# Optimization experiments

Measured on AMD Instinct MI355X. Metric: run time of the kernel, lower is better.

Reference implementation:

```python
import jax, jax.numpy as jnp
import numpy as np

N_NODES = 100000
N_EDGES = 6400000

def setup_inputs() -> dict:
    key = jax.random.key(0)
    ks = jax.random.split(key, 12)
    x = jax.random.normal(ks[0], (N_NODES, 2), dtype=jnp.float32)
    edge_index = jax.random.randint(ks[1], (2, N_EDGES), 0, N_NODES, dtype=jnp.int32)
    def w(k, fi, fo):
        return jax.random.normal(k, (fi, fo), dtype=jnp.float32) * (1.0 / np.sqrt(fi))
    return {
        "x": x, "edge_index": edge_index,
        "W0": w(ks[2], 2, 8), "b0": jnp.zeros((8,), jnp.float32),
        "W1": w(ks[3], 8, 8), "b1": jnp.zeros((8,), jnp.float32),
        "W2": w(ks[4], 8, 8), "b2": jnp.zeros((8,), jnp.float32),
        "W3": w(ks[5], 8, 8), "b3": jnp.zeros((8,), jnp.float32),
        "Wv": w(ks[6], 8, 1), "bv": jnp.zeros((1,), jnp.float32),
        "Wp": w(ks[7], 8, 1), "bp": jnp.zeros((1,), jnp.float32),
    }

def _gcn_norm(edge_index, n_nodes):
    # PyG GCNConv default: add self-loops, symmetric D^{-1/2} A_hat D^{-1/2}
    loops = jnp.arange(n_nodes, dtype=edge_index.dtype)
    src = jnp.concatenate([edge_index[0], loops])
    dst = jnp.concatenate([edge_index[1], loops])
    deg = jax.ops.segment_sum(jnp.ones_like(dst, dtype=jnp.float32), dst,
                              num_segments=n_nodes)
    dis = jax.lax.rsqrt(jnp.maximum(deg, 1.0))  # deg >= 1 due to self-loops
    norm = dis[src] * dis[dst]                   # [E + N]
    return src, dst, norm

def _gcn_conv(x, W, b, src, dst, norm, n_nodes):
    h = x @ W                                     # small GEMM [N, fo]
    msg = h[src] * norm[:, None]                  # gather + normalize
    out = jax.ops.segment_sum(msg, dst, num_segments=n_nodes)  # scatter-add
    return out + b

def reference(x, edge_index, W0, b0, W1, b1, W2, b2, W3, b3, Wv, bv, Wp, bp):
    n = x.shape[0]
    src, dst, norm = _gcn_norm(edge_index, n)
    h = x
    for W, b in ((W0, b0), (W1, b1), (W2, b2), (W3, b3)):
        h = jax.nn.elu(_gcn_conv(h, W, b, src, dst, norm, n))
    mean_val = _gcn_conv(h, Wv, bv, src, dst, norm, n)   # [N, 1]
    value = jnp.mean(mean_val, axis=0, keepdims=True)    # global_mean_pool, 1 graph -> [1, 1]
    proba = _gcn_conv(h, Wp, bp, src, dst, norm, n)      # [N, 1]
    return (proba, value)
```

## Files before the change

### kernel.cpp

```cpp
#include <hip/hip_runtime.h>

#define NT 256
#define CHUNK 1024
#define PBLK2 2048
#define PTILE 4096

static inline int nbi(long long n) { return (int)((n + NT - 1) / NT); }


__global__ __launch_bounds__(256) void k_histB(const int* __restrict__ dst,
                                               int* __restrict__ histB,
                                               int E, int NB) {
    __shared__ int lh[512];
    int t = threadIdx.x;
    for (int i = t; i < 512; i += 256) lh[i] = 0;
    __syncthreads();
    int chunk = (E + gridDim.x - 1) / gridDim.x;
    int lo = blockIdx.x * chunk, hi = min(E, lo + chunk);
    for (int i = lo + t; i < hi; i += 256)
        atomicAdd(&lh[dst[i] >> 8], 1);
    __syncthreads();
    for (int b = t; b < NB; b += 256)
        histB[(size_t)blockIdx.x * NB + b] = lh[b];
}

__global__ __launch_bounds__(256) void k_scanB2(const int* __restrict__ histB,
                                                int* __restrict__ cursorT,
                                                int* __restrict__ tot,
                                                int NB, int nblk) {
    __shared__ int ch[256];
    __shared__ int carry;
    int b = blockIdx.x, t = threadIdx.x;
    if (t == 0) carry = 0;
    __syncthreads();
    for (int c = 0; c < nblk; c += 256) {
        int blk = c + t;
        int v = (blk < nblk) ? histB[(size_t)blk * NB + b] : 0;
        ch[t] = v;
        __syncthreads();
        for (int o = 1; o < 256; o <<= 1) {
            int x = (t >= o) ? ch[t - o] : 0;
            __syncthreads();
            ch[t] += x;
            __syncthreads();
        }
        int excl = ch[t] - v + carry;
        if (blk < nblk) cursorT[(size_t)b * PBLK2 + blk] = excl;
        __syncthreads();
        if (t == 0) carry += ch[255];
        __syncthreads();
    }
    if (t == 0) tot[b] = carry;
}

__global__ __launch_bounds__(512) void k_bscan(const int* __restrict__ hist_g,
                                               int* __restrict__ bbase,
                                               int* __restrict__ cursor,
                                               int* __restrict__ rowst,
                                               int NB, int N, int E) {
    __shared__ int s[512];
    int t = threadIdx.x;
    int own = (t < NB) ? hist_g[t] : 0;
    s[t] = own;
    __syncthreads();
    for (int o = 1; o < 512; o <<= 1) {
        int v = (t >= o) ? s[t - o] : 0;
        __syncthreads();
        s[t] += v;
        __syncthreads();
    }
    if (t < NB) { int ex = s[t] - own; bbase[t] = ex; cursor[t] = ex; }
    if (t == 0) { bbase[NB] = E; rowst[N] = E; }
}

__global__ __launch_bounds__(256) void k_partF(const int* __restrict__ src,
                                               const int* __restrict__ dst,
                                               const int* __restrict__ bbase,
                                               const int* __restrict__ cursorT,
                                               int* __restrict__ part,
                                               int E, int NB) {
    __shared__ int wcur[512];
    __shared__ int th[512], tloff[512], tcnt[512];
    __shared__ int ps[256];
    __shared__ int stage[PTILE];
    __shared__ unsigned short sbkt[PTILE];
    int t = threadIdx.x;
    int chunk = (E + gridDim.x - 1) / gridDim.x;
    int lo = blockIdx.x * chunk, hi = min(E, lo + chunk);
    if (lo >= hi) return;

    for (int b = t; b < NB; b += 256)
        wcur[b] = bbase[b] + cursorT[(size_t)b * PBLK2 + blockIdx.x];
    __syncthreads();

    for (int tlo = lo; tlo < hi; tlo += PTILE) {
        int thi = min(hi, tlo + PTILE);
        int cnt = thi - tlo;
        for (int i = t; i < 512; i += 256) { th[i] = 0; tcnt[i] = 0; }
        __syncthreads();
        for (int i = tlo + t; i < thi; i += 256) atomicAdd(&th[dst[i] >> 8], 1);
        __syncthreads();
        int a0 = th[2 * t], a1 = th[2 * t + 1];
        int psum = a0 + a1;
        ps[t] = psum;
        __syncthreads();
        for (int o = 1; o < 256; o <<= 1) {
            int v = (t >= o) ? ps[t - o] : 0;
            __syncthreads();
            ps[t] += v;
            __syncthreads();
        }
        int excl = ps[t] - psum;
        tloff[2 * t] = excl;
        tloff[2 * t + 1] = excl + a0;
        __syncthreads();
        for (int i = tlo + t; i < thi; i += 256) {
            int d = dst[i], s = src[i];
            int b = d >> 8;
            int pos = tloff[b] + atomicAdd(&tcnt[b], 1);
            stage[pos] = ((d & 255) << 17) | s;
            sbkt[pos] = (unsigned short)b;
        }
        __syncthreads();
        for (int i = t; i < cnt; i += 256) {
            int b = sbkt[i];
            part[wcur[b] + (i - tloff[b])] = stage[i];
        }
        __syncthreads();
        for (int b = t; b < NB; b += 256) wcur[b] += th[b];
        __syncthreads();
    }
}

__global__ __launch_bounds__(512) void k_build(const int* __restrict__ bbase,
                                               const int* __restrict__ part,
                                               int* __restrict__ rowst,
                                               float* __restrict__ dis,
                                               int* __restrict__ csr,
                                               int N) {
    __shared__ int dcnt[256], doff[256];
    int b = blockIdx.x, t = threadIdx.x;
    int lo = bbase[b], hi = bbase[b + 1];
    if (t < 256) dcnt[t] = 0;
    __syncthreads();
    for (int i = lo + t; i < hi; i += 512)
        atomicAdd(&dcnt[part[i] >> 17], 1);
    __syncthreads();
    int own = 0;
    if (t < 256) { own = dcnt[t]; doff[t] = own; }
    __syncthreads();
    for (int o = 1; o < 256; o <<= 1) {
        int v = 0;
        if (t < 256 && t >= o) v = doff[t - o];
        __syncthreads();
        if (t < 256) doff[t] += v;
        __syncthreads();
    }
    if (t < 256) {
        int excl = doff[t] - own;
        int node = (b << 8) + t;
        if (node < N) {
            rowst[node] = lo + excl;
            dis[node] = rsqrtf((float)own + 1.0f);
        }
        dcnt[t] = excl;
    }
    __syncthreads();
    for (int i = lo + t; i < hi; i += 512) {
        int pv = part[i];
        int slot = atomicAdd(&dcnt[pv >> 17], 1);
        csr[lo + slot] = pv & 0x1FFFF;
    }
}


__global__ __launch_bounds__(NT) void k_node0n(const float* __restrict__ x,
                                               const float* __restrict__ W,
                                               const float* __restrict__ dis,
                                               float* __restrict__ u, int N) {
    int n = blockIdx.x * NT + threadIdx.x;
    if (n >= N) return;
    float2 xv = *reinterpret_cast<const float2*>(x + 2 * n);
    float dn = dis[n];
    float o[8];
#pragma unroll
    for (int f = 0; f < 8; ++f) o[f] = dn * (xv.x * W[f] + xv.y * W[8 + f]);
    float4* up = reinterpret_cast<float4*>(u + 8 * n);
    up[0] = make_float4(o[0], o[1], o[2], o[3]);
    up[1] = make_float4(o[4], o[5], o[6], o[7]);
}

#define GATHER8_BODY(IDX)                                                     \
    {                                                                         \
        float4 p0 = *reinterpret_cast<const float4*>(u + 8 * (IDX));          \
        float4 p1 = *reinterpret_cast<const float4*>(u + 8 * (IDX) + 4);      \
        a[0] += p0.x; a[1] += p0.y; a[2] += p0.z; a[3] += p0.w;               \
        a[4] += p1.x; a[5] += p1.y; a[6] += p1.z; a[7] += p1.w;               \
    }

__global__ __launch_bounds__(NT) void k_gather_layer(const int* __restrict__ rowst,
                                                     const int* __restrict__ csr,
                                                     const float* __restrict__ dis,
                                                     const float* __restrict__ u,
                                                     const float* __restrict__ b,
                                                     const float* __restrict__ W,
                                                     float* __restrict__ un, int N) {
    int g = blockIdx.x * NT + threadIdx.x;
    int n = g >> 2, sub = g & 3;
    if (n >= N) return;
    int i = rowst[n] + sub, end = rowst[n + 1];
    float a[8];
#pragma unroll
    for (int k = 0; k < 8; ++k) a[k] = 0.0f;
    int s0 = 0, s1 = 0, s2 = 0, s3 = 0;
    bool run4 = (i + 12 < end);
    if (run4) { s0 = csr[i]; s1 = csr[i + 4]; s2 = csr[i + 8]; s3 = csr[i + 12]; }
    while (run4) {
        int ni = i + 16;
        bool nrun = (ni + 12 < end);
        int t0 = 0, t1 = 0, t2 = 0, t3 = 0;
        if (nrun) { t0 = csr[ni]; t1 = csr[ni + 4]; t2 = csr[ni + 8]; t3 = csr[ni + 12]; }
        GATHER8_BODY(s0); GATHER8_BODY(s1); GATHER8_BODY(s2); GATHER8_BODY(s3);
        i = ni; run4 = nrun; s0 = t0; s1 = t1; s2 = t2; s3 = t3;
    }
    for (; i + 4 < end; i += 8) {
        int q0 = csr[i], q1 = csr[i + 4];
        GATHER8_BODY(q0); GATHER8_BODY(q1);
    }
    if (i < end) { int q0 = csr[i]; GATHER8_BODY(q0); }
#pragma unroll
    for (int k = 0; k < 8; ++k) {
        a[k] += __shfl_xor(a[k], 1, 64);
        a[k] += __shfl_xor(a[k], 2, 64);
    }
    float va = sub == 0 ? a[0] : (sub == 1 ? a[2] : (sub == 2 ? a[4] : a[6]));
    float vb = sub == 0 ? a[1] : (sub == 1 ? a[3] : (sub == 2 ? a[5] : a[7]));
    float2 selfv = *reinterpret_cast<const float2*>(u + 8 * n + 2 * sub);
    va += selfv.x; vb += selfv.y;
    float dn = dis[n];
    float2 bb = *reinterpret_cast<const float2*>(b + 2 * sub);
    float g0 = va * dn + bb.x, g1 = vb * dn + bb.y;
    float h0 = g0 > 0.0f ? g0 : expm1f(g0);
    float h1 = g1 > 0.0f ? g1 : expm1f(g1);
    int base = (threadIdx.x & 63) & ~3;
    float hh0 = __shfl(h0, base + 0, 64), hh1 = __shfl(h1, base + 0, 64);
    float hh2 = __shfl(h0, base + 1, 64), hh3 = __shfl(h1, base + 1, 64);
    float hh4 = __shfl(h0, base + 2, 64), hh5 = __shfl(h1, base + 2, 64);
    float hh6 = __shfl(h0, base + 3, 64), hh7 = __shfl(h1, base + 3, 64);
    int fo = 2 * sub;
    float o0 = hh0 * W[0 * 8 + fo] + hh1 * W[1 * 8 + fo] + hh2 * W[2 * 8 + fo] +
               hh3 * W[3 * 8 + fo] + hh4 * W[4 * 8 + fo] + hh5 * W[5 * 8 + fo] +
               hh6 * W[6 * 8 + fo] + hh7 * W[7 * 8 + fo];
    float o1 = hh0 * W[0 * 8 + fo + 1] + hh1 * W[1 * 8 + fo + 1] + hh2 * W[2 * 8 + fo + 1] +
               hh3 * W[3 * 8 + fo + 1] + hh4 * W[4 * 8 + fo + 1] + hh5 * W[5 * 8 + fo + 1] +
               hh6 * W[6 * 8 + fo + 1] + hh7 * W[7 * 8 + fo + 1];
    *reinterpret_cast<float2*>(un + 8 * n + fo) = make_float2(dn * o0, dn * o1);
}

__global__ __launch_bounds__(NT) void k_gather_head(const int* __restrict__ rowst,
                                                    const int* __restrict__ csr,
                                                    const float* __restrict__ dis,
                                                    const float* __restrict__ u,
                                                    const float* __restrict__ b,
                                                    const float* __restrict__ Wv,
                                                    const float* __restrict__ Wp,
                                                    float* __restrict__ uH, int N) {
    int g = blockIdx.x * NT + threadIdx.x;
    int n = g >> 2, sub = g & 3;
    if (n >= N) return;
    int i = rowst[n] + sub, end = rowst[n + 1];
    float a[8];
#pragma unroll
    for (int k = 0; k < 8; ++k) a[k] = 0.0f;
    int s0 = 0, s1 = 0, s2 = 0, s3 = 0;
    bool run4 = (i + 12 < end);
    if (run4) { s0 = csr[i]; s1 = csr[i + 4]; s2 = csr[i + 8]; s3 = csr[i + 12]; }
    while (run4) {
        int ni = i + 16;
        bool nrun = (ni + 12 < end);
        int t0 = 0, t1 = 0, t2 = 0, t3 = 0;
        if (nrun) { t0 = csr[ni]; t1 = csr[ni + 4]; t2 = csr[ni + 8]; t3 = csr[ni + 12]; }
        GATHER8_BODY(s0); GATHER8_BODY(s1); GATHER8_BODY(s2); GATHER8_BODY(s3);
        i = ni; run4 = nrun; s0 = t0; s1 = t1; s2 = t2; s3 = t3;
    }
    for (; i + 4 < end; i += 8) {
        int q0 = csr[i], q1 = csr[i + 4];
        GATHER8_BODY(q0); GATHER8_BODY(q1);
    }
    if (i < end) { int q0 = csr[i]; GATHER8_BODY(q0); }
#pragma unroll
    for (int k = 0; k < 8; ++k) {
        a[k] += __shfl_xor(a[k], 1, 64);
        a[k] += __shfl_xor(a[k], 2, 64);
    }
    float va = sub == 0 ? a[0] : (sub == 1 ? a[2] : (sub == 2 ? a[4] : a[6]));
    float vb = sub == 0 ? a[1] : (sub == 1 ? a[3] : (sub == 2 ? a[5] : a[7]));
    float2 selfv = *reinterpret_cast<const float2*>(u + 8 * n + 2 * sub);
    va += selfv.x; vb += selfv.y;
    float dn = dis[n];
    float2 bb = *reinterpret_cast<const float2*>(b + 2 * sub);
    float g0 = va * dn + bb.x, g1 = vb * dn + bb.y;
    float h0 = g0 > 0.0f ? g0 : expm1f(g0);
    float h1 = g1 > 0.0f ? g1 : expm1f(g1);
    float tvp = h0 * Wv[2 * sub] + h1 * Wv[2 * sub + 1];
    float tpp = h0 * Wp[2 * sub] + h1 * Wp[2 * sub + 1];
    tvp += __shfl_xor(tvp, 1, 64); tvp += __shfl_xor(tvp, 2, 64);
    tpp += __shfl_xor(tpp, 1, 64); tpp += __shfl_xor(tpp, 2, 64);
    if (sub == 0)
        *reinterpret_cast<float2*>(uH + 2 * n) = make_float2(dn * tvp, dn * tpp);
}

__global__ __launch_bounds__(NT) void k_gather2n(const int* __restrict__ rowst,
                                                 const int* __restrict__ csr,
                                                 const float* __restrict__ dis,
                                                 const float* __restrict__ uH,
                                                 const float* __restrict__ bp,
                                                 float* __restrict__ out,
                                                 float* __restrict__ vsum, int N) {
    int g = blockIdx.x * NT + threadIdx.x;
    int n = g >> 2, sub = g & 3;
    bool valid = n < N;
    int i = 0, end = 0;
    if (valid) { i = rowst[n] + sub; end = rowst[n + 1]; }
    float av = 0.0f, ap = 0.0f;
    int s0 = 0, s1 = 0, s2 = 0, s3 = 0;
    bool run4 = (i + 12 < end);
    if (run4) { s0 = csr[i]; s1 = csr[i + 4]; s2 = csr[i + 8]; s3 = csr[i + 12]; }
    while (run4) {
        int ni = i + 16;
        bool nrun = (ni + 12 < end);
        int t0 = 0, t1 = 0, t2 = 0, t3 = 0;
        if (nrun) { t0 = csr[ni]; t1 = csr[ni + 4]; t2 = csr[ni + 8]; t3 = csr[ni + 12]; }
        float2 p0 = *reinterpret_cast<const float2*>(uH + 2 * s0);
        float2 p1 = *reinterpret_cast<const float2*>(uH + 2 * s1);
        float2 p2 = *reinterpret_cast<const float2*>(uH + 2 * s2);
        float2 p3 = *reinterpret_cast<const float2*>(uH + 2 * s3);
        av += p0.x + p1.x + p2.x + p3.x;
        ap += p0.y + p1.y + p2.y + p3.y;
        i = ni; run4 = nrun; s0 = t0; s1 = t1; s2 = t2; s3 = t3;
    }
    for (; i + 4 < end; i += 8) {
        int q0 = csr[i], q1 = csr[i + 4];
        float2 p = *reinterpret_cast<const float2*>(uH + 2 * q0);
        float2 q = *reinterpret_cast<const float2*>(uH + 2 * q1);
        av += p.x + q.x; ap += p.y + q.y;
    }
    if (i < end) {
        int q0 = csr[i];
        float2 p = *reinterpret_cast<const float2*>(uH + 2 * q0);
        av += p.x; ap += p.y;
    }
    av += __shfl_xor(av, 1, 64); av += __shfl_xor(av, 2, 64);
    ap += __shfl_xor(ap, 1, 64); ap += __shfl_xor(ap, 2, 64);
    float contrib = 0.0f;
    if (valid && sub == 0) {
        float2 selfv = *reinterpret_cast<const float2*>(uH + 2 * n);
        av += selfv.x; ap += selfv.y;
        float dn = dis[n];
        out[n] = ap * dn + bp[0];
        contrib = av * dn;
    }
#pragma unroll
    for (int o = 32; o > 0; o >>= 1) contrib += __shfl_down(contrib, o, 64);
    __shared__ float sred[NT / 64];
    if ((threadIdx.x & 63) == 0) sred[threadIdx.x >> 6] = contrib;
    __syncthreads();
    if (threadIdx.x == 0) {
        float bsum = 0.0f;
#pragma unroll
        for (int k = 0; k < NT / 64; ++k) bsum += sred[k];
        atomicAdd(vsum, bsum);
    }
}

__global__ void k_final(const float* __restrict__ vsum,
                        const float* __restrict__ bv,
                        float* __restrict__ out, int N) {
    out[0] = vsum[0] * (1.0f / (float)N) + bv[0];
}


__global__ __launch_bounds__(NT) void k_count(const int* __restrict__ dst,
                                              int* __restrict__ deg, int E) {
    int e = blockIdx.x * NT + threadIdx.x;
    if (e < E) atomicAdd(&deg[dst[e]], 1);
}

__global__ __launch_bounds__(NT) void k_scanA(const int* __restrict__ deg,
                                              int* __restrict__ partial, int N) {
    int t = threadIdx.x;
    int base = blockIdx.x * CHUNK + t * 4;
    int s = 0;
#pragma unroll
    for (int j = 0; j < 4; ++j) { int i = base + j; if (i < N) s += deg[i]; }
    __shared__ int red[NT];
    red[t] = s; __syncthreads();
    for (int o = NT / 2; o > 0; o >>= 1) {
        if (t < o) red[t] += red[t + o];
        __syncthreads();
    }
    if (t == 0) partial[blockIdx.x] = red[0];
}

__global__ void k_scanB(const int* __restrict__ partial, int* __restrict__ chunkoff,
                        int* __restrict__ rowst, int nblk, int N) {
    if (threadIdx.x == 0) {
        int off = 0;
        for (int b = 0; b < nblk; ++b) { chunkoff[b] = off; off += partial[b]; }
        rowst[N] = off;
    }
}

__global__ __launch_bounds__(NT) void k_scanC(const int* __restrict__ deg,
                                              const int* __restrict__ chunkoff,
                                              int* __restrict__ rowst,
                                              float* __restrict__ dis, int N) {
    int t = threadIdx.x;
    int base = blockIdx.x * CHUNK + t * 4;
    int v[4]; int tsum = 0;
#pragma unroll
    for (int j = 0; j < 4; ++j) { int i = base + j; v[j] = (i < N) ? deg[i] : 0; tsum += v[j]; }
    __shared__ int ss[NT];
    ss[t] = tsum; __syncthreads();
    for (int o = 1; o < NT; o <<= 1) {
        int x = (t >= o) ? ss[t - o] : 0;
        __syncthreads();
        ss[t] += x;
        __syncthreads();
    }
    int run = ss[t] - tsum + chunkoff[blockIdx.x];
#pragma unroll
    for (int j = 0; j < 4; ++j) {
        int i = base + j;
        if (i < N) { rowst[i] = run; dis[i] = rsqrtf((float)v[j] + 1.0f); run += v[j]; }
    }
}

__global__ __launch_bounds__(NT) void k_fill(const int* __restrict__ src,
                                             const int* __restrict__ dst,
                                             const int* __restrict__ rowst,
                                             int* __restrict__ deg,
                                             int* __restrict__ csr, int E) {
    int e = blockIdx.x * NT + threadIdx.x;
    if (e >= E) return;
    int s = src[e], d = dst[e];
    int old = atomicSub(&deg[d], 1);
    csr[rowst[d] + old - 1] = s;
}


extern "C" void kernel_launch(void* const* d_in, const int* in_sizes, int n_in,
                              void* d_out, int out_size, void* d_ws, size_t ws_size,
                              hipStream_t stream) {
    const float* x  = (const float*)d_in[0];
    const int* ei   = (const int*)d_in[1];
    const float* W0 = (const float*)d_in[2];
    const float* b0 = (const float*)d_in[3];
    const float* W1 = (const float*)d_in[4];
    const float* b1 = (const float*)d_in[5];
    const float* W2 = (const float*)d_in[6];
    const float* b2 = (const float*)d_in[7];
    const float* W3 = (const float*)d_in[8];
    const float* b3 = (const float*)d_in[9];
    const float* Wv = (const float*)d_in[10];
    const float* bv = (const float*)d_in[11];
    const float* Wp = (const float*)d_in[12];
    const float* bp = (const float*)d_in[13];
    float* out = (float*)d_out;

    int N = in_sizes[0] / 2;
    int E = in_sizes[1] / 2;
    const int* src = ei;
    const int* dst = ei + E;
    int NB = (N + 255) >> 8;

    size_t needP = ((size_t)18 * N + 2 * (size_t)E + 2048) * 4;
    bool histFits = (size_t)2 * PBLK2 * NB <= (size_t)E;

    if (N <= 131072 && NB <= 512 && ws_size >= needP && histFits) {
        int* tot    = (int*)d_ws;
        int* bbase  = tot + 512;
        float* vsum = (float*)(bbase + 513);
        int* rowst  = (int*)(vsum + 8);
        float* dis  = (float*)(rowst + N + 1);
        float* uA   = dis + N;
        float* uB   = uA + (size_t)8 * N;
        int* part   = (int*)(uB + (size_t)8 * N);
        int* csr    = part + (size_t)E;
        int* histB   = csr;
        int* cursorT = csr + (size_t)PBLK2 * NB;

        hipMemsetAsync(vsum, 0, 4, stream);

        k_histB<<<PBLK2, 256, 0, stream>>>(dst, histB, E, NB);
        k_scanB2<<<NB, 256, 0, stream>>>(histB, cursorT, tot, NB, PBLK2);
        k_bscan<<<1, 512, 0, stream>>>(tot, bbase, tot, rowst, NB, N, E);
        k_partF<<<PBLK2, 256, 0, stream>>>(src, dst, bbase, cursorT, part, E, NB);
        k_build<<<NB, 512, 0, stream>>>(bbase, part, rowst, dis, csr, N);

        k_node0n<<<nbi(N), NT, 0, stream>>>(x, W0, dis, uA, N);
        k_gather_layer<<<nbi(4LL * N), NT, 0, stream>>>(rowst, csr, dis, uA, b0, W1, uB, N);
        k_gather_layer<<<nbi(4LL * N), NT, 0, stream>>>(rowst, csr, dis, uB, b1, W2, uA, N);
        k_gather_layer<<<nbi(4LL * N), NT, 0, stream>>>(rowst, csr, dis, uA, b2, W3, uB, N);
        k_gather_head<<<nbi(4LL * N), NT, 0, stream>>>(rowst, csr, dis, uB, b3, Wv, Wp, uA, N);
        k_gather2n<<<nbi(4LL * N), NT, 0, stream>>>(rowst, csr, dis, uA, bp, out, vsum, N);
        k_final<<<1, 1, 0, stream>>>(vsum, bv, out + N, N);
    } else {
        int nblk = (N + CHUNK - 1) / CHUNK;
        int* deg      = (int*)d_ws;
        int* rowst    = deg + N;
        int* chunkoff = rowst + N + 1;
        int* partial  = chunkoff + nblk;
        float* dis    = (float*)(partial + nblk);
        float* vsum   = dis + N;
        float* uA     = vsum + 8;
        float* uB     = uA + (size_t)8 * N;
        int* csr      = (int*)(uB + (size_t)8 * N);

        hipMemsetAsync(deg, 0, (size_t)N * 4, stream);
        hipMemsetAsync(vsum, 0, 4, stream);

        k_count<<<nbi(E), NT, 0, stream>>>(dst, deg, E);
        k_scanA<<<nblk, NT, 0, stream>>>(deg, partial, N);
        k_scanB<<<1, 64, 0, stream>>>(partial, chunkoff, rowst, nblk, N);
        k_scanC<<<nblk, NT, 0, stream>>>(deg, chunkoff, rowst, dis, N);
        k_fill<<<nbi(E), NT, 0, stream>>>(src, dst, rowst, deg, csr, E);

        k_node0n<<<nbi(N), NT, 0, stream>>>(x, W0, dis, uA, N);
        k_gather_layer<<<nbi(4LL * N), NT, 0, stream>>>(rowst, csr, dis, uA, b0, W1, uB, N);
        k_gather_layer<<<nbi(4LL * N), NT, 0, stream>>>(rowst, csr, dis, uB, b1, W2, uA, N);
        k_gather_layer<<<nbi(4LL * N), NT, 0, stream>>>(rowst, csr, dis, uA, b2, W3, uB, N);
        k_gather_head<<<nbi(4LL * N), NT, 0, stream>>>(rowst, csr, dis, uB, b3, Wv, Wp, uA, N);
        k_gather2n<<<nbi(4LL * N), NT, 0, stream>>>(rowst, csr, dis, uA, bp, out, vsum, N);
        k_final<<<1, 1, 0, stream>>>(vsum, bv, out + N, N);
    }
}
```

Before: 376.3 us.

## Aggregate raw 2-wide input first, widen gathers to 8 lanes per node

The first layer now aggregates the 2-feature normalized input (dis*x) before applying W0, so its gather reads 8 bytes per edge instead of 32. The dis*x prescale is folded into the CSR build kernel, which removes the separate node-transform launch. All gather kernels move from 4 to 8 lanes per node with a simpler two-deep prefetch and a transpose-style shuffle reduction, so each lane ends up owning one output feature. The head output also gets its own buffer. This raises thread count and shuffle work, and the shorter per-lane loops may hide memory latency less well.

```diff
diff --git a/kernel.cpp b/kernel.cpp
--- a/kernel.cpp
+++ b/kernel.cpp
@@ -55,7 +55,6 @@
 
 __global__ __launch_bounds__(512) void k_bscan(const int* __restrict__ hist_g,
                                                int* __restrict__ bbase,
-                                               int* __restrict__ cursor,
                                                int* __restrict__ rowst,
                                                int NB, int N, int E) {
     __shared__ int s[512];
@@ -69,7 +68,7 @@
         s[t] += v;
         __syncthreads();
     }
-    if (t < NB) { int ex = s[t] - own; bbase[t] = ex; cursor[t] = ex; }
+    if (t < NB) bbase[t] = s[t] - own;
     if (t == 0) { bbase[NB] = E; rowst[N] = E; }
 }
 
@@ -134,8 +133,10 @@
 
 __global__ __launch_bounds__(512) void k_build(const int* __restrict__ bbase,
                                                const int* __restrict__ part,
+                                               const float* __restrict__ x,
                                                int* __restrict__ rowst,
                                                float* __restrict__ dis,
+                                               float* __restrict__ v0,
                                                int* __restrict__ csr,
                                                int N) {
     __shared__ int dcnt[256], doff[256];
@@ -161,7 +162,10 @@
         int node = (b << 8) + t;
         if (node < N) {
             rowst[node] = lo + excl;
-            dis[node] = rsqrtf((float)own + 1.0f);
+            float dn = rsqrtf((float)own + 1.0f);
+            dis[node] = dn;
+            float2 xv = *reinterpret_cast<const float2*>(x + 2 * node);
+            *reinterpret_cast<float2*>(v0 + 2 * node) = make_float2(dn * xv.x, dn * xv.y);
         }
         dcnt[t] = excl;
     }
@@ -174,184 +178,188 @@
 }
 
 
-__global__ __launch_bounds__(NT) void k_node0n(const float* __restrict__ x,
-                                               const float* __restrict__ W,
-                                               const float* __restrict__ dis,
-                                               float* __restrict__ u, int N) {
-    int n = blockIdx.x * NT + threadIdx.x;
+__global__ __launch_bounds__(NT) void k_gL1(const int* __restrict__ rowst,
+                                            const int* __restrict__ csr,
+                                            const float* __restrict__ dis,
+                                            const float* __restrict__ v0,
+                                            const float* __restrict__ W0,
+                                            const float* __restrict__ b0,
+                                            const float* __restrict__ W1,
+                                            float* __restrict__ un, int N) {
+    int g = blockIdx.x * NT + threadIdx.x;
+    int n = g >> 3, sub = g & 7;
     if (n >= N) return;
-    float2 xv = *reinterpret_cast<const float2*>(x + 2 * n);
+    int i = rowst[n] + sub, end = rowst[n + 1];
+    float ax = 0.0f, ay = 0.0f;
+    int s0 = 0, s1 = 0;
+    bool r0 = i < end, r1 = i + 8 < end;
+    if (r0) s0 = csr[i];
+    if (r1) s1 = csr[i + 8];
+    while (r0) {
+        float2 p = *reinterpret_cast<const float2*>(v0 + 2 * s0);
+        int i2 = i + 16;
+        bool r2 = i2 < end;
+        int s2 = 0; if (r2) s2 = csr[i2];
+        ax += p.x; ay += p.y;
+        i += 8; r0 = r1; s0 = s1; r1 = r2; s1 = s2;
+    }
+    ax += __shfl_xor(ax, 1, 64); ax += __shfl_xor(ax, 2, 64); ax += __shfl_xor(ax, 4, 64);
+    ay += __shfl_xor(ay, 1, 64); ay += __shfl_xor(ay, 2, 64); ay += __shfl_xor(ay, 4, 64);
+    float2 sv = *reinterpret_cast<const float2*>(v0 + 2 * n);
+    ax += sv.x; ay += sv.y;
     float dn = dis[n];
-    float o[8];
-#pragma unroll
-    for (int f = 0; f < 8; ++f) o[f] = dn * (xv.x * W[f] + xv.y * W[8 + f]);
-    float4* up = reinterpret_cast<float4*>(u + 8 * n);
-    up[0] = make_float4(o[0], o[1], o[2], o[3]);
-    up[1] = make_float4(o[4], o[5], o[6], o[7]);
-}
-
-#define GATHER8_BODY(IDX)                                                     \
-    {                                                                         \
-        float4 p0 = *reinterpret_cast<const float4*>(u + 8 * (IDX));          \
-        float4 p1 = *reinterpret_cast<const float4*>(u + 8 * (IDX) + 4);      \
-        a[0] += p0.x; a[1] += p0.y; a[2] += p0.z; a[3] += p0.w;               \
-        a[4] += p1.x; a[5] += p1.y; a[6] += p1.z; a[7] += p1.w;               \
-    }
-
-__global__ __launch_bounds__(NT) void k_gather_layer(const int* __restrict__ rowst,
-                                                     const int* __restrict__ csr,
-                                                     const float* __restrict__ dis,
-                                                     const float* __restrict__ u,
-                                                     const float* __restrict__ b,
-                                                     const float* __restrict__ W,
-                                                     float* __restrict__ un, int N) {
+    float gg = dn * (ax * W0[sub] + ay * W0[8 + sub]) + b0[sub];
+    float h = gg > 0.0f ? gg : expm1f(gg);
+    int base = (threadIdx.x & 63) & ~7;
+    float o = 0.0f;
+#pragma unroll
+    for (int k = 0; k < 8; ++k) o += __shfl(h, base + k, 64) * W1[k * 8 + sub];
+    un[8 * n + sub] = dn * o;
+}
+
+__global__ __launch_bounds__(NT) void k_gL8(const int* __restrict__ rowst,
+                                            const int* __restrict__ csr,
+                                            const float* __restrict__ dis,
+                                            const float* __restrict__ u,
+                                            const float* __restrict__ b,
+                                            const float* __restrict__ W,
+                                            float* __restrict__ un, int N) {
     int g = blockIdx.x * NT + threadIdx.x;
-    int n = g >> 2, sub = g & 3;
+    int n = g >> 3, sub = g & 7;
     if (n >= N) return;
     int i = rowst[n] + sub, end = rowst[n + 1];
     float a[8];
 #pragma unroll
     for (int k = 0; k < 8; ++k) a[k] = 0.0f;
-    int s0 = 0, s1 = 0, s2 = 0, s3 = 0;
-    bool run4 = (i + 12 < end);
-    if (run4) { s0 = csr[i]; s1 = csr[i + 4]; s2 = csr[i + 8]; s3 = csr[i + 12]; }
-    while (run4) {
-        int ni = i + 16;
-        bool nrun = (ni + 12 < end);
-        int t0 = 0, t1 = 0, t2 = 0, t3 = 0;
-        if (nrun) { t0 = csr[ni]; t1 = csr[ni + 4]; t2 = csr[ni + 8]; t3 = csr[ni + 12]; }
-        GATHER8_BODY(s0); GATHER8_BODY(s1); GATHER8_BODY(s2); GATHER8_BODY(s3);
-        i = ni; run4 = nrun; s0 = t0; s1 = t1; s2 = t2; s3 = t3;
-    }
-    for (; i + 4 < end; i += 8) {
-        int q0 = csr[i], q1 = csr[i + 4];
-        GATHER8_BODY(q0); GATHER8_BODY(q1);
-    }
-    if (i < end) { int q0 = csr[i]; GATHER8_BODY(q0); }
-#pragma unroll
-    for (int k = 0; k < 8; ++k) {
-        a[k] += __shfl_xor(a[k], 1, 64);
-        a[k] += __shfl_xor(a[k], 2, 64);
-    }
-    float va = sub == 0 ? a[0] : (sub == 1 ? a[2] : (sub == 2 ? a[4] : a[6]));
-    float vb = sub == 0 ? a[1] : (sub == 1 ? a[3] : (sub == 2 ? a[5] : a[7]));
-    float2 selfv = *reinterpret_cast<const float2*>(u + 8 * n + 2 * sub);
-    va += selfv.x; vb += selfv.y;
+    int s0 = 0, s1 = 0;
+    bool r0 = i < end, r1 = i + 8 < end;
+    if (r0) s0 = csr[i];
+    if (r1) s1 = csr[i + 8];
+    while (r0) {
+        float4 p0 = *reinterpret_cast<const float4*>(u + 8 * s0);
+        float4 p1 = *reinterpret_cast<const float4*>(u + 8 * s0 + 4);
+        int i2 = i + 16;
+        bool r2 = i2 < end;
+        int s2 = 0; if (r2) s2 = csr[i2];
+        a[0] += p0.x; a[1] += p0.y; a[2] += p0.z; a[3] += p0.w;
+        a[4] += p1.x; a[5] += p1.y; a[6] += p1.z; a[7] += p1.w;
+        i += 8; r0 = r1; s0 = s1; r1 = r2; s1 = s2;
+    }
+    int c4 = sub & 4, c2 = sub & 2, c1 = sub & 1;
+#pragma unroll
+    for (int j = 0; j < 4; ++j) {
+        float send = c4 ? a[j] : a[j + 4];
+        float recv = __shfl_xor(send, 4, 64);
+        a[j] = (c4 ? a[j + 4] : a[j]) + recv;
+    }
+#pragma unroll
+    for (int j = 0; j < 2; ++j) {
+        float send = c2 ? a[j] : a[j + 2];
+        float recv = __shfl_xor(send, 2, 64);
+        a[j] = (c2 ? a[j + 2] : a[j]) + recv;
+    }
+    {
+        float send = c1 ? a[0] : a[1];
+        float recv = __shfl_xor(send, 1, 64);
+        a[0] = (c1 ? a[1] : a[0]) + recv;
+    }
     float dn = dis[n];
-    float2 bb = *reinterpret_cast<const float2*>(b + 2 * sub);
-    float g0 = va * dn + bb.x, g1 = vb * dn + bb.y;
-    float h0 = g0 > 0.0f ? g0 : expm1f(g0);
-    float h1 = g1 > 0.0f ? g1 : expm1f(g1);
-    int base = (threadIdx.x & 63) & ~3;
-    float hh0 = __shfl(h0, base + 0, 64), hh1 = __shfl(h1, base + 0, 64);
-    float hh2 = __shfl(h0, base + 1, 64), hh3 = __shfl(h1, base + 1, 64);
-    float hh4 = __shfl(h0, base + 2, 64), hh5 = __shfl(h1, base + 2, 64);
-    float hh6 = __shfl(h0, base + 3, 64), hh7 = __shfl(h1, base + 3, 64);
-    int fo = 2 * sub;
-    float o0 = hh0 * W[0 * 8 + fo] + hh1 * W[1 * 8 + fo] + hh2 * W[2 * 8 + fo] +
-               hh3 * W[3 * 8 + fo] + hh4 * W[4 * 8 + fo] + hh5 * W[5 * 8 + fo] +
-               hh6 * W[6 * 8 + fo] + hh7 * W[7 * 8 + fo];
-    float o1 = hh0 * W[0 * 8 + fo + 1] + hh1 * W[1 * 8 + fo + 1] + hh2 * W[2 * 8 + fo + 1] +
-               hh3 * W[3 * 8 + fo + 1] + hh4 * W[4 * 8 + fo + 1] + hh5 * W[5 * 8 + fo + 1] +
-               hh6 * W[6 * 8 + fo + 1] + hh7 * W[7 * 8 + fo + 1];
-    *reinterpret_cast<float2*>(un + 8 * n + fo) = make_float2(dn * o0, dn * o1);
-}
-
-__global__ __launch_bounds__(NT) void k_gather_head(const int* __restrict__ rowst,
-                                                    const int* __restrict__ csr,
-                                                    const float* __restrict__ dis,
-                                                    const float* __restrict__ u,
-                                                    const float* __restrict__ b,
-                                                    const float* __restrict__ Wv,
-                                                    const float* __restrict__ Wp,
-                                                    float* __restrict__ uH, int N) {
+    float va = a[0] + u[8 * n + sub];
+    float gg = va * dn + b[sub];
+    float h = gg > 0.0f ? gg : expm1f(gg);
+    int base = (threadIdx.x & 63) & ~7;
+    float o = 0.0f;
+#pragma unroll
+    for (int k = 0; k < 8; ++k) o += __shfl(h, base + k, 64) * W[k * 8 + sub];
+    un[8 * n + sub] = dn * o;
+}
+
+__global__ __launch_bounds__(NT) void k_gHead(const int* __restrict__ rowst,
+                                              const int* __restrict__ csr,
+                                              const float* __restrict__ dis,
+                                              const float* __restrict__ u,
+                                              const float* __restrict__ b,
+                                              const float* __restrict__ Wv,
+                                              const float* __restrict__ Wp,
+                                              float* __restrict__ uH, int N) {
     int g = blockIdx.x * NT + threadIdx.x;
-    int n = g >> 2, sub = g & 3;
+    int n = g >> 3, sub = g & 7;
     if (n >= N) return;
     int i = rowst[n] + sub, end = rowst[n + 1];
     float a[8];
 #pragma unroll
     for (int k = 0; k < 8; ++k) a[k] = 0.0f;
-    int s0 = 0, s1 = 0, s2 = 0, s3 = 0;
-    bool run4 = (i + 12 < end);
-    if (run4) { s0 = csr[i]; s1 = csr[i + 4]; s2 = csr[i + 8]; s3 = csr[i + 12]; }
-    while (run4) {
-        int ni = i + 16;
-        bool nrun = (ni + 12 < end);
-        int t0 = 0, t1 = 0, t2 = 0, t3 = 0;
-        if (nrun) { t0 = csr[ni]; t1 = csr[ni + 4]; t2 = csr[ni + 8]; t3 = csr[ni + 12]; }
-        GATHER8_BODY(s0); GATHER8_BODY(s1); GATHER8_BODY(s2); GATHER8_BODY(s3);
-        i = ni; run4 = nrun; s0 = t0; s1 = t1; s2 = t2; s3 = t3;
-    }
-    for (; i + 4 < end; i += 8) {
-        int q0 = csr[i], q1 = csr[i + 4];
-        GATHER8_BODY(q0); GATHER8_BODY(q1);
-    }
-    if (i < end) { int q0 = csr[i]; GATHER8_BODY(q0); }
-#pragma unroll
-    for (int k = 0; k < 8; ++k) {
-        a[k] += __shfl_xor(a[k], 1, 64);
-        a[k] += __shfl_xor(a[k], 2, 64);
-    }
-    float va = sub == 0 ? a[0] : (sub == 1 ? a[2] : (sub == 2 ? a[4] : a[6]));
-    float vb = sub == 0 ? a[1] : (sub == 1 ? a[3] : (sub == 2 ? a[5] : a[7]));
-    float2 selfv = *reinterpret_cast<const float2*>(u + 8 * n + 2 * sub);
-    va += selfv.x; vb += selfv.y;
+    int s0 = 0, s1 = 0;
+    bool r0 = i < end, r1 = i + 8 < end;
+    if (r0) s0 = csr[i];
+    if (r1) s1 = csr[i + 8];
+    while (r0) {
+        float4 p0 = *reinterpret_cast<const float4*>(u + 8 * s0);
+        float4 p1 = *reinterpret_cast<const float4*>(u + 8 * s0 + 4);
+        int i2 = i + 16;
+        bool r2 = i2 < end;
+        int s2 = 0; if (r2) s2 = csr[i2];
+        a[0] += p0.x; a[1] += p0.y; a[2] += p0.z; a[3] += p0.w;
+        a[4] += p1.x; a[5] += p1.y; a[6] += p1.z; a[7] += p1.w;
+        i += 8; r0 = r1; s0 = s1; r1 = r2; s1 = s2;
+    }
+    int c4 = sub & 4, c2 = sub & 2, c1 = sub & 1;
+#pragma unroll
+    for (int j = 0; j < 4; ++j) {
+        float send = c4 ? a[j] : a[j + 4];
+        float recv = __shfl_xor(send, 4, 64);
+        a[j] = (c4 ? a[j + 4] : a[j]) + recv;
+    }
+#pragma unroll
+    for (int j = 0; j < 2; ++j) {
+        float send = c2 ? a[j] : a[j + 2];
+        float recv = __shfl_xor(send, 2, 64);
+        a[j] = (c2 ? a[j + 2] : a[j]) + recv;
+    }
+    {
+        float send = c1 ? a[0] : a[1];
+        float recv = __shfl_xor(send, 1, 64);
+        a[0] = (c1 ? a[1] : a[0]) + recv;
+    }
     float dn = dis[n];
-    float2 bb = *reinterpret_cast<const float2*>(b + 2 * sub);
-    float g0 = va * dn + bb.x, g1 = vb * dn + bb.y;
-    float h0 = g0 > 0.0f ? g0 : expm1f(g0);
-    float h1 = g1 > 0.0f ? g1 : expm1f(g1);
-    float tvp = h0 * Wv[2 * sub] + h1 * Wv[2 * sub + 1];
-    float tpp = h0 * Wp[2 * sub] + h1 * Wp[2 * sub + 1];
-    tvp += __shfl_xor(tvp, 1, 64); tvp += __shfl_xor(tvp, 2, 64);
-    tpp += __shfl_xor(tpp, 1, 64); tpp += __shfl_xor(tpp, 2, 64);
+    float va = a[0] + u[8 * n + sub];
+    float gg = va * dn + b[sub];
+    float h = gg > 0.0f ? gg : expm1f(gg);
+    float tv = h * Wv[sub];
+    float tp = h * Wp[sub];
+    tv += __shfl_xor(tv, 1, 64); tv += __shfl_xor(tv, 2, 64); tv += __shfl_xor(tv, 4, 64);
+    tp += __shfl_xor(tp, 1, 64); tp += __shfl_xor(tp, 2, 64); tp += __shfl_xor(tp, 4, 64);
     if (sub == 0)
-        *reinterpret_cast<float2*>(uH + 2 * n) = make_float2(dn * tvp, dn * tpp);
-}
-
-__global__ __launch_bounds__(NT) void k_gather2n(const int* __restrict__ rowst,
-                                                 const int* __restrict__ csr,
-                                                 const float* __restrict__ dis,
-                                                 const float* __restrict__ uH,
-                                                 const float* __restrict__ bp,
-                                                 float* __restrict__ out,
-                                                 float* __restrict__ vsum, int N) {
+        *reinterpret_cast<float2*>(uH + 2 * n) = make_float2(dn * tv, dn * tp);
+}
+
+__global__ __launch_bounds__(NT) void k_g2F(const int* __restrict__ rowst,
+                                            const int* __restrict__ csr,
+                                            const float* __restrict__ dis,
+                                            const float* __restrict__ uH,
+                                            const float* __restrict__ bp,
+                                            float* __restrict__ out,
+                                            float* __restrict__ vsum, int N) {
     int g = blockIdx.x * NT + threadIdx.x;
-    int n = g >> 2, sub = g & 3;
+    int n = g >> 3, sub = g & 7;
     bool valid = n < N;
     int i = 0, end = 0;
     if (valid) { i = rowst[n] + sub; end = rowst[n + 1]; }
     float av = 0.0f, ap = 0.0f;
-    int s0 = 0, s1 = 0, s2 = 0, s3 = 0;
-    bool run4 = (i + 12 < end);
-    if (run4) { s0 = csr[i]; s1 = csr[i + 4]; s2 = csr[i + 8]; s3 = csr[i + 12]; }
-    while (run4) {
-        int ni = i + 16;
-        bool nrun = (ni + 12 < end);
-        int t0 = 0, t1 = 0, t2 = 0, t3 = 0;
-        if (nrun) { t0 = csr[ni]; t1 = csr[ni + 4]; t2 = csr[ni + 8]; t3 = csr[ni + 12]; }
-        float2 p0 = *reinterpret_cast<const float2*>(uH + 2 * s0);
-        float2 p1 = *reinterpret_cast<const float2*>(uH + 2 * s1);
-        float2 p2 = *reinterpret_cast<const float2*>(uH + 2 * s2);
-        float2 p3 = *reinterpret_cast<const float2*>(uH + 2 * s3);
-        av += p0.x + p1.x + p2.x + p3.x;
-        ap += p0.y + p1.y + p2.y + p3.y;
-        i = ni; run4 = nrun; s0 = t0; s1 = t1; s2 = t2; s3 = t3;
-    }
-    for (; i + 4 < end; i += 8) {
-        int q0 = csr[i], q1 = csr[i + 4];
-        float2 p = *reinterpret_cast<const float2*>(uH + 2 * q0);
-        float2 q = *reinterpret_cast<const float2*>(uH + 2 * q1);
-        av += p.x + q.x; ap += p.y + q.y;
-    }
-    if (i < end) {
-        int q0 = csr[i];
-        float2 p = *reinterpret_cast<const float2*>(uH + 2 * q0);
+    int s0 = 0, s1 = 0;
+    bool r0 = i < end, r1 = i + 8 < end;
+    if (r0) s0 = csr[i];
+    if (r1) s1 = csr[i + 8];
+    while (r0) {
+        float2 p = *reinterpret_cast<const float2*>(uH + 2 * s0);
+        int i2 = i + 16;
+        bool r2 = i2 < end;
+        int s2 = 0; if (r2) s2 = csr[i2];
         av += p.x; ap += p.y;
-    }
-    av += __shfl_xor(av, 1, 64); av += __shfl_xor(av, 2, 64);
-    ap += __shfl_xor(ap, 1, 64); ap += __shfl_xor(ap, 2, 64);
+        i = i + 8; r0 = r1; s0 = s1; r1 = r2; s1 = s2;
+    }
+    av += __shfl_xor(av, 1, 64); av += __shfl_xor(av, 2, 64); av += __shfl_xor(av, 4, 64);
+    ap += __shfl_xor(ap, 1, 64); ap += __shfl_xor(ap, 2, 64); ap += __shfl_xor(ap, 4, 64);
     float contrib = 0.0f;
     if (valid && sub == 0) {
         float2 selfv = *reinterpret_cast<const float2*>(uH + 2 * n);
@@ -446,6 +454,16 @@
     int s = src[e], d = dst[e];
     int old = atomicSub(&deg[d], 1);
     csr[rowst[d] + old - 1] = s;
+}
+
+__global__ __launch_bounds__(NT) void k_v0(const float* __restrict__ x,
+                                           const float* __restrict__ dis,
+                                           float* __restrict__ v0, int N) {
+    int n = blockIdx.x * NT + threadIdx.x;
+    if (n >= N) return;
+    float dn = dis[n];
+    float2 xv = *reinterpret_cast<const float2*>(x + 2 * n);
+    *reinterpret_cast<float2*>(v0 + 2 * n) = make_float2(dn * xv.x, dn * xv.y);
 }
 
 
@@ -474,7 +492,7 @@
     const int* dst = ei + E;
     int NB = (N + 255) >> 8;
 
-    size_t needP = ((size_t)18 * N + 2 * (size_t)E + 2048) * 4;
+    size_t needP = ((size_t)22 * N + 2 * (size_t)E + 2048) * 4;
     bool histFits = (size_t)2 * PBLK2 * NB <= (size_t)E;
 
     if (N <= 131072 && NB <= 512 && ws_size >= needP && histFits) {
@@ -483,9 +501,11 @@
         float* vsum = (float*)(bbase + 513);
         int* rowst  = (int*)(vsum + 8);
         float* dis  = (float*)(rowst + N + 1);
-        float* uA   = dis + N;
+        float* v0   = dis + N;
+        float* uA   = v0 + (size_t)2 * N;
         float* uB   = uA + (size_t)8 * N;
-        int* part   = (int*)(uB + (size_t)8 * N);
+        float* uH   = uB + (size_t)8 * N;
+        int* part   = (int*)(uH + (size_t)2 * N);
         int* csr    = part + (size_t)E;
         int* histB   = csr;
         int* cursorT = csr + (size_t)PBLK2 * NB;
@@ -494,16 +514,15 @@
 
         k_histB<<<PBLK2, 256, 0, stream>>>(dst, histB, E, NB);
         k_scanB2<<<NB, 256, 0, stream>>>(histB, cursorT, tot, NB, PBLK2);
-        k_bscan<<<1, 512, 0, stream>>>(tot, bbase, tot, rowst, NB, N, E);
+        k_bscan<<<1, 512, 0, stream>>>(tot, bbase, rowst, NB, N, E);
         k_partF<<<PBLK2, 256, 0, stream>>>(src, dst, bbase, cursorT, part, E, NB);
-        k_build<<<NB, 512, 0, stream>>>(bbase, part, rowst, dis, csr, N);
-
-        k_node0n<<<nbi(N), NT, 0, stream>>>(x, W0, dis, uA, N);
-        k_gather_layer<<<nbi(4LL * N), NT, 0, stream>>>(rowst, csr, dis, uA, b0, W1, uB, N);
-        k_gather_layer<<<nbi(4LL * N), NT, 0, stream>>>(rowst, csr, dis, uB, b1, W2, uA, N);
-        k_gather_layer<<<nbi(4LL * N), NT, 0, stream>>>(rowst, csr, dis, uA, b2, W3, uB, N);
-        k_gather_head<<<nbi(4LL * N), NT, 0, stream>>>(rowst, csr, dis, uB, b3, Wv, Wp, uA, N);
-        k_gather2n<<<nbi(4LL * N), NT, 0, stream>>>(rowst, csr, dis, uA, bp, out, vsum, N);
+        k_build<<<NB, 512, 0, stream>>>(bbase, part, x, rowst, dis, v0, csr, N);
+
+        k_gL1<<<nbi(8LL * N), NT, 0, stream>>>(rowst, csr, dis, v0, W0, b0, W1, uA, N);
+        k_gL8<<<nbi(8LL * N), NT, 0, stream>>>(rowst, csr, dis, uA, b1, W2, uB, N);
+        k_gL8<<<nbi(8LL * N), NT, 0, stream>>>(rowst, csr, dis, uB, b2, W3, uA, N);
+        k_gHead<<<nbi(8LL * N), NT, 0, stream>>>(rowst, csr, dis, uA, b3, Wv, Wp, uH, N);
+        k_g2F<<<nbi(8LL * N), NT, 0, stream>>>(rowst, csr, dis, uH, bp, out, vsum, N);
         k_final<<<1, 1, 0, stream>>>(vsum, bv, out + N, N);
     } else {
         int nblk = (N + CHUNK - 1) / CHUNK;
@@ -513,9 +532,11 @@
         int* partial  = chunkoff + nblk;
         float* dis    = (float*)(partial + nblk);
         float* vsum   = dis + N;
-        float* uA     = vsum + 8;
+        float* v0     = vsum + 8;
+        float* uA     = v0 + (size_t)2 * N;
         float* uB     = uA + (size_t)8 * N;
-        int* csr      = (int*)(uB + (size_t)8 * N);
+        float* uH     = uB + (size_t)8 * N;
+        int* csr      = (int*)(uH + (size_t)2 * N);
 
         hipMemsetAsync(deg, 0, (size_t)N * 4, stream);
         hipMemsetAsync(vsum, 0, 4, stream);
@@ -525,13 +546,13 @@
         k_scanB<<<1, 64, 0, stream>>>(partial, chunkoff, rowst, nblk, N);
         k_scanC<<<nblk, NT, 0, stream>>>(deg, chunkoff, rowst, dis, N);
         k_fill<<<nbi(E), NT, 0, stream>>>(src, dst, rowst, deg, csr, E);
-
-        k_node0n<<<nbi(N), NT, 0, stream>>>(x, W0, dis, uA, N);
-        k_gather_layer<<<nbi(4LL * N), NT, 0, stream>>>(rowst, csr, dis, uA, b0, W1, uB, N);
-        k_gather_layer<<<nbi(4LL * N), NT, 0, stream>>>(rowst, csr, dis, uB, b1, W2, uA, N);
-        k_gather_layer<<<nbi(4LL * N), NT, 0, stream>>>(rowst, csr, dis, uA, b2, W3, uB, N);
-        k_gather_head<<<nbi(4LL * N), NT, 0, stream>>>(rowst, csr, dis, uB, b3, Wv, Wp, uA, N);
-        k_gather2n<<<nbi(4LL * N), NT, 0, stream>>>(rowst, csr, dis, uA, bp, out, vsum, N);
+        k_v0<<<nbi(N), NT, 0, stream>>>(x, dis, v0, N);
+
+        k_gL1<<<nbi(8LL * N), NT, 0, stream>>>(rowst, csr, dis, v0, W0, b0, W1, uA, N);
+        k_gL8<<<nbi(8LL * N), NT, 0, stream>>>(rowst, csr, dis, uA, b1, W2, uB, N);
+        k_gL8<<<nbi(8LL * N), NT, 0, stream>>>(rowst, csr, dis, uB, b2, W3, uA, N);
+        k_gHead<<<nbi(8LL * N), NT, 0, stream>>>(rowst, csr, dis, uA, b3, Wv, Wp, uH, N);
+        k_g2F<<<nbi(8LL * N), NT, 0, stream>>>(rowst, csr, dis, uH, bp, out, vsum, N);
         k_final<<<1, 1, 0, stream>>>(vsum, bv, out + N, N);
     }
 }
```

Result: faster. 355.8 us (-5.4%).
